# Kernel optimization log

Measured on AMD Instinct MI355X. Metric: run time of the kernel, lower is better.

## Reference

```python
import jax, jax.numpy as jnp
import numpy as np

LAMBDA_COOR = 5.0
LAMBDA_NOOBJ = 0.5


def setup_inputs() -> dict:
    key = jax.random.key(0)
    k1, k2 = jax.random.split(key)
    B, W, H, C = 128, 256, 256, 5
    outputs = jax.random.normal(k1, (B, W, H, C), dtype=jnp.float32)
    targets = jax.random.normal(k2, (B, W, H, C), dtype=jnp.float32)
    return {"outputs": outputs, "targets": targets}


def reference(outputs, targets):
    # channel layout per cell: (conf, x, y, w, h)
    conf_pred = outputs[..., 0]
    conf_gt = targets[..., 0]
    obj_mask = conf_gt > 0
    # sum of squared coord errors (x, y, w, h) per cell: [B, W, H]
    coord_sq = jnp.sum((outputs[..., 1:] - targets[..., 1:]) ** 2, axis=-1)
    obj_loss = LAMBDA_COOR * coord_sq + (conf_pred - 1.0) ** 2
    noobj_loss = LAMBDA_NOOBJ * conf_pred ** 2
    loss = jnp.sum(jnp.where(obj_mask, obj_loss, noobj_loss))
    return loss / outputs.shape[0]
```

## Files before the change

kernel.cpp:

```cpp
#include <hip/hip_runtime.h>

#define LAMBDA_COOR 5.0f
#define LAMBDA_NOOBJ 0.5f

__global__ __launch_bounds__(256) void yolo_loss_kernel(
    const float* __restrict__ outp, const float* __restrict__ tgt,
    float* __restrict__ loss, int n_groups, float inv_b)
{
    int tid = blockIdx.x * blockDim.x + threadIdx.x;
    int stride = gridDim.x * blockDim.x;
    float acc = 0.0f;

    for (int g = tid; g < n_groups; g += stride) {
        const float4* o4 = (const float4*)(outp + (size_t)g * 20);
        const float4* t4 = (const float4*)(tgt + (size_t)g * 20);
        float o[20], t[20];
        #pragma unroll
        for (int i = 0; i < 5; ++i) {
            float4 a = o4[i];
            float4 b = t4[i];
            o[4*i+0] = a.x; o[4*i+1] = a.y; o[4*i+2] = a.z; o[4*i+3] = a.w;
            t[4*i+0] = b.x; t[4*i+1] = b.y; t[4*i+2] = b.z; t[4*i+3] = b.w;
        }
        #pragma unroll
        for (int c = 0; c < 4; ++c) {
            const float* oc = o + 5*c;
            const float* tc = t + 5*c;
            float conf_p = oc[0];
            float coord = 0.0f;
            #pragma unroll
            for (int k = 1; k < 5; ++k) {
                float d = oc[k] - tc[k];
                coord += d * d;
            }
            float obj   = LAMBDA_COOR * coord + (conf_p - 1.0f) * (conf_p - 1.0f);
            float noobj = LAMBDA_NOOBJ * conf_p * conf_p;
            acc += (tc[0] > 0.0f) ? obj : noobj;
        }
    }

    #pragma unroll
    for (int off = 32; off > 0; off >>= 1)
        acc += __shfl_down(acc, off, 64);

    __shared__ float wave_sums[4];
    int lane = threadIdx.x & 63;
    int wid  = threadIdx.x >> 6;
    if (lane == 0) wave_sums[wid] = acc;
    __syncthreads();

    if (threadIdx.x == 0) {
        float s = wave_sums[0] + wave_sums[1] + wave_sums[2] + wave_sums[3];
        atomicAdd(loss, s * inv_b);
    }
}

extern "C" void kernel_launch(void* const* d_in, const int* in_sizes, int n_in,
                              void* d_out, int out_size, void* d_ws, size_t ws_size,
                              hipStream_t stream) {
    const float* outputs = (const float*)d_in[0];
    const float* targets = (const float*)d_in[1];
    float* loss = (float*)d_out;

    const int n_elems  = in_sizes[0];
    const int n_groups = n_elems / 20;
    const float inv_b  = 1.0f / 128.0f;

    hipMemsetAsync(d_out, 0, sizeof(float), stream);

    const int threads = 256;
    const int blocks  = 2048;
    yolo_loss_kernel<<<blocks, threads, 0, stream>>>(
        outputs, targets, loss, n_groups, inv_b);
}
```

Before: 332.9 us.

## Coalesce per-wave float4 loads and restage cells through LDS

Measured after the change: 335.2 us. No clear change (+0.7%).

```diff
diff --git a/kernel.cpp b/kernel.cpp
--- a/kernel.cpp
+++ b/kernel.cpp
@@ -3,38 +3,58 @@
 #define LAMBDA_COOR 5.0f
 #define LAMBDA_NOOBJ 0.5f
 
-__global__ __launch_bounds__(256) void yolo_loss_kernel(
-    const float* __restrict__ outp, const float* __restrict__ tgt,
-    float* __restrict__ loss, int n_groups, float inv_b)
+constexpr int TPB = 256;
+constexpr int WAVES_PER_BLOCK = TPB / 64;
+constexpr int WAVE_F4 = 5 * 64;
+constexpr int WAVE_FLOATS = WAVE_F4 * 4;
+
+__global__ __launch_bounds__(TPB) void yolo_loss_kernel(
+    const float4* __restrict__ outp4, const float4* __restrict__ tgt4,
+    float* __restrict__ loss, int n_wtiles, float inv_b)
 {
-    int tid = blockIdx.x * blockDim.x + threadIdx.x;
-    int stride = gridDim.x * blockDim.x;
+    __shared__ float so[WAVES_PER_BLOCK][WAVE_FLOATS];
+    __shared__ float st[WAVES_PER_BLOCK][WAVE_FLOATS];
+
+    const int lane  = threadIdx.x & 63;
+    const int wid   = threadIdx.x >> 6;
+    const int gwave = blockIdx.x * WAVES_PER_BLOCK + wid;
+    const int nwaves = gridDim.x * WAVES_PER_BLOCK;
+
     float acc = 0.0f;
 
-    for (int g = tid; g < n_groups; g += stride) {
-        const float4* o4 = (const float4*)(outp + (size_t)g * 20);
-        const float4* t4 = (const float4*)(tgt + (size_t)g * 20);
-        float o[20], t[20];
+    for (int w = gwave; w < n_wtiles; w += nwaves) {
+        const size_t base4 = (size_t)w * WAVE_F4;
+
+        float4 vo[5], vt[5];
         #pragma unroll
-        for (int i = 0; i < 5; ++i) {
-            float4 a = o4[i];
-            float4 b = t4[i];
-            o[4*i+0] = a.x; o[4*i+1] = a.y; o[4*i+2] = a.z; o[4*i+3] = a.w;
-            t[4*i+0] = b.x; t[4*i+1] = b.y; t[4*i+2] = b.z; t[4*i+3] = b.w;
+        for (int k = 0; k < 5; ++k) {
+            vo[k] = outp4[base4 + (size_t)(k * 64 + lane)];
+            vt[k] = tgt4 [base4 + (size_t)(k * 64 + lane)];
         }
+
+        float4* so4 = (float4*)so[wid];
+        float4* st4 = (float4*)st[wid];
+        #pragma unroll
+        for (int k = 0; k < 5; ++k) {
+            so4[k * 64 + lane] = vo[k];
+            st4[k * 64 + lane] = vt[k];
+        }
+
+        const float* o = &so[wid][20 * lane];
+        const float* t = &st[wid][20 * lane];
         #pragma unroll
         for (int c = 0; c < 4; ++c) {
-            const float* oc = o + 5*c;
-            const float* tc = t + 5*c;
-            float conf_p = oc[0];
+            const float* oc = o + 5 * c;
+            const float* tc = t + 5 * c;
+            float conf = oc[0];
             float coord = 0.0f;
             #pragma unroll
             for (int k = 1; k < 5; ++k) {
                 float d = oc[k] - tc[k];
-                coord += d * d;
+                coord = fmaf(d, d, coord);
             }
-            float obj   = LAMBDA_COOR * coord + (conf_p - 1.0f) * (conf_p - 1.0f);
-            float noobj = LAMBDA_NOOBJ * conf_p * conf_p;
+            float obj   = fmaf(LAMBDA_COOR, coord, (conf - 1.0f) * (conf - 1.0f));
+            float noobj = LAMBDA_NOOBJ * conf * conf;
             acc += (tc[0] > 0.0f) ? obj : noobj;
         }
     }
@@ -43,14 +63,14 @@
     for (int off = 32; off > 0; off >>= 1)
         acc += __shfl_down(acc, off, 64);
 
-    __shared__ float wave_sums[4];
-    int lane = threadIdx.x & 63;
-    int wid  = threadIdx.x >> 6;
+    __shared__ float wave_sums[WAVES_PER_BLOCK];
     if (lane == 0) wave_sums[wid] = acc;
     __syncthreads();
 
     if (threadIdx.x == 0) {
-        float s = wave_sums[0] + wave_sums[1] + wave_sums[2] + wave_sums[3];
+        float s = 0.0f;
+        #pragma unroll
+        for (int i = 0; i < WAVES_PER_BLOCK; ++i) s += wave_sums[i];
         atomicAdd(loss, s * inv_b);
     }
 }
@@ -58,18 +78,17 @@
 extern "C" void kernel_launch(void* const* d_in, const int* in_sizes, int n_in,
                               void* d_out, int out_size, void* d_ws, size_t ws_size,
                               hipStream_t stream) {
-    const float* outputs = (const float*)d_in[0];
-    const float* targets = (const float*)d_in[1];
+    const float4* outputs = (const float4*)d_in[0];
+    const float4* targets = (const float4*)d_in[1];
     float* loss = (float*)d_out;
 
     const int n_elems  = in_sizes[0];
-    const int n_groups = n_elems / 20;
+    const int n_wtiles = n_elems / WAVE_FLOATS;
     const float inv_b  = 1.0f / 128.0f;
 
     hipMemsetAsync(d_out, 0, sizeof(float), stream);
 
-    const int threads = 256;
-    const int blocks  = 2048;
-    yolo_loss_kernel<<<blocks, threads, 0, stream>>>(
-        outputs, targets, loss, n_groups, inv_b);
+    const int blocks = 2048;
+    yolo_loss_kernel<<<blocks, TPB, 0, stream>>>(
+        outputs, targets, loss, n_wtiles, inv_b);
 }
```
